# Optimization experiments

Hardware: AMD Instinct MI355X
Metric: run time of the kernel (lower is better)

## Reference

```python
import jax, jax.numpy as jnp
import numpy as np

B, L, H, E, FF, TOPK = 2, 2048, 1024, 8, 4096, 2

def setup_inputs() -> dict:
    key = jax.random.key(0)
    k1, k2, k3, k4 = jax.random.split(key, 4)
    scale = 1.0 / np.sqrt(H)
    x = jax.random.normal(k1, (B, L, H), dtype=jnp.float32)
    Wg = jax.random.normal(k2, (H, E), dtype=jnp.float32) * scale
    Wfc = jax.random.normal(k3, (E, H, FF), dtype=jnp.float32) * scale
    Wproj = jax.random.normal(k4, (E, FF, H), dtype=jnp.float32) * (1.0 / np.sqrt(FF))
    return {"x": x, "Wg": Wg, "Wfc": Wfc, "Wproj": Wproj, "topk": TOPK}

def reference(x, Wg, Wfc, Wproj, topk):
    b, l, h = x.shape
    e = Wg.shape[1]
    xf = x.reshape(-1, h)                      # [T, h]
    T = xf.shape[0]
    # --- router: softmax over experts, top-k select, renormalize ---
    probs = jax.nn.softmax(xf @ Wg, axis=-1)   # [T, E]
    sel_w, sel_e = jax.lax.top_k(probs, topk)  # [T, k]
    sel_w = sel_w / jnp.sum(sel_w, axis=-1, keepdims=True)
    # dense per-token expert weight matrix [T, E] (0 for unselected experts)
    dense_w = jnp.zeros((T, e), dtype=x.dtype).at[jnp.arange(T)[:, None], sel_e].add(sel_w)
    # --- experts: relu(x Wfc)^2 Wproj, combined with routing weights ---
    h1 = jnp.einsum('th,ehf->etf', xf, Wfc)    # [E, T, FF]
    h1 = jnp.square(jax.nn.relu(h1))
    y = jnp.einsum('etf,efh->eth', h1, Wproj)  # [E, T, h]
    out = jnp.einsum('eth,te->th', y, dense_w) # weighted combine
    return out.reshape(b, l, h)
```

## Files before the change

### kernel.cpp

```cpp
#include <hip/hip_runtime.h>

#define T_TOK 4096
#define HDIM  1024
#define NEXP  8
#define FFDIM 4096
#define NPAIR 8192
#define MAXMT 72

typedef __attribute__((ext_vector_type(8))) short short8;
typedef __attribute__((ext_vector_type(8))) unsigned short ushort8;
typedef __attribute__((ext_vector_type(4))) unsigned short ushort4_t;
typedef __attribute__((ext_vector_type(4))) float f32x4;

__device__ __forceinline__ unsigned short f2bf(float f) {
  unsigned int u = __float_as_uint(f);
  u += 0x7fffu + ((u >> 16) & 1u);
  return (unsigned short)(u >> 16);
}
__device__ __forceinline__ float bf2f(unsigned short u) {
  return __uint_as_float((unsigned int)u << 16);
}

__device__ __forceinline__ void gload16(const void* g, const void* l) {
  __builtin_amdgcn_global_load_lds(
      (const __attribute__((address_space(1))) unsigned int*)(unsigned long long)g,
      (__attribute__((address_space(3))) unsigned int*)(unsigned int)(unsigned long long)l,
      16, 0, 0);
}

__device__ __forceinline__ void transpose_tile_256(
    const float* __restrict__ in, unsigned short* __restrict__ out,
    int M, int N, int my, int nx, unsigned short* t , int tid) {
  int r0 = my * 256, c0 = nx * 64;
  int colb = (tid & 15) * 4;
  int rowi = tid >> 4;
  int sw = (tid & 7) << 3;
#pragma unroll
  for (int i = 0; i < 16; i++) {
    int row = i * 16 + rowi;
    float4 v = *(const float4*)(in + (size_t)(r0 + row) * N + c0 + colb);
    int rs = row ^ sw;
    t[(colb + 0) * 264 + rs] = f2bf(v.x);
    t[(colb + 1) * 264 + rs] = f2bf(v.y);
    t[(colb + 2) * 264 + rs] = f2bf(v.z);
    t[(colb + 3) * 264 + rs] = f2bf(v.w);
  }
  __syncthreads();
  int m0 = (tid & 31) * 8;
  int nsub = tid >> 5;
#pragma unroll
  for (int i = 0; i < 8; i++) {
    int n = i * 8 + nsub;
    int sn = ((n >> 2) & 7) << 3;
    ushort8 v = *(const ushort8*)&t[n * 264 + (m0 ^ sn)];
    *(ushort8*)(out + (size_t)(c0 + n) * M + r0 + m0) = v;
  }
}

__global__ __launch_bounds__(256) void routerA_kernel(
    const float* __restrict__ x, const float* __restrict__ wg,
    unsigned short* __restrict__ xb,
    int* __restrict__ sel_e, float* __restrict__ sel_w,
    const float* __restrict__ Wfc, unsigned short* __restrict__ WfcT) {
  __shared__ unsigned short tbuf[64 * 264];
  int id = blockIdx.x;
  if (id >= 1024) {
    int b = id - 1024;
    int e = b >> 8, r = b & 255;
    transpose_tile_256(Wfc + (size_t)e * HDIM * FFDIM, WfcT + (size_t)e * HDIM * FFDIM,
                       HDIM, FFDIM, r >> 6, r & 63, tbuf, threadIdx.x);
    return;
  }
  int lane = threadIdx.x & 63;
  int t = id * 4 + (threadIdx.x >> 6);
  const float* xr = x + (size_t)t * HDIM;
  unsigned short* xo = xb + (size_t)t * HDIM;
  float acc[8] = {0, 0, 0, 0, 0, 0, 0, 0};
#pragma unroll
  for (int i = 0; i < 4; i++) {
    int h0 = i * 256 + lane * 4;
    float4 xv = *(const float4*)(xr + h0);
    *(ushort4_t*)(xo + h0) = (ushort4_t){f2bf(xv.x), f2bf(xv.y), f2bf(xv.z), f2bf(xv.w)};
    float xs[4] = {xv.x, xv.y, xv.z, xv.w};
#pragma unroll
    for (int k = 0; k < 4; k++) {
      const float* wr_ = wg + (size_t)(h0 + k) * 8;
      float4 w0 = *(const float4*)(wr_);
      float4 w1 = *(const float4*)(wr_ + 4);
      acc[0] += xs[k] * w0.x; acc[1] += xs[k] * w0.y; acc[2] += xs[k] * w0.z; acc[3] += xs[k] * w0.w;
      acc[4] += xs[k] * w1.x; acc[5] += xs[k] * w1.y; acc[6] += xs[k] * w1.z; acc[7] += xs[k] * w1.w;
    }
  }
#pragma unroll
  for (int off = 32; off > 0; off >>= 1) {
#pragma unroll
    for (int e = 0; e < 8; e++) acc[e] += __shfl_xor(acc[e], off, 64);
  }
  if (lane == 0) {
    int e0 = 0; float b0 = acc[0];
#pragma unroll
    for (int e = 1; e < 8; e++) if (acc[e] > b0) { b0 = acc[e]; e0 = e; }
    int e1 = -1; float b1 = -3.4e38f;
#pragma unroll
    for (int e = 0; e < 8; e++) if (e != e0 && acc[e] > b1) { b1 = acc[e]; e1 = e; }
    float q = expf(b1 - b0);
    float w0 = 1.0f / (1.0f + q);
    float w1 = q / (1.0f + q);
    sel_e[t * 2] = e0; sel_e[t * 2 + 1] = e1;
    sel_w[t * 2] = w0; sel_w[t * 2 + 1] = w1;
  }
}

__global__ __launch_bounds__(1024) void count_scatter_kernel(
    const int* __restrict__ sel_e, int* __restrict__ counts,
    int* __restrict__ pair_token, int* __restrict__ pair_pos) {
  __shared__ int wtot[16][NEXP];
  __shared__ int wcur[16][NEXP];
  int tid = threadIdx.x;
  int wv = tid >> 6;
  int lane = tid & 63;
  int4 a = *(const int4*)(sel_e + tid * 8);
  int4 b = *(const int4*)(sel_e + tid * 8 + 4);
  int es[8] = {a.x, a.y, a.z, a.w, b.x, b.y, b.z, b.w};
  int c[NEXP] = {0, 0, 0, 0, 0, 0, 0, 0};
#pragma unroll
  for (int j = 0; j < 8; j++) c[es[j]]++;
#pragma unroll
  for (int off = 32; off > 0; off >>= 1)
#pragma unroll
    for (int e = 0; e < NEXP; e++) c[e] += __shfl_xor(c[e], off, 64);
  if (lane == 0)
#pragma unroll
    for (int e = 0; e < NEXP; e++) wtot[wv][e] = c[e];
  __syncthreads();
  if (tid == 0) {
    int tot[NEXP];
#pragma unroll
    for (int e = 0; e < NEXP; e++) {
      int s = 0;
      for (int w2 = 0; w2 < 16; w2++) s += wtot[w2][e];
      tot[e] = s;
    }
    int s = 0;
    for (int e = 0; e < NEXP; e++) {
      counts[e] = tot[e];
      int base = s;
      for (int w2 = 0; w2 < 16; w2++) { wcur[w2][e] = base; base += wtot[w2][e]; }
      s += tot[e];
    }
  }
  __syncthreads();
#pragma unroll
  for (int j = 0; j < 8; j++) {
    int e = es[j];
    int pos = atomicAdd(&wcur[wv][e], 1);
    int entry = tid * 8 + j;
    pair_token[pos] = entry >> 1;
    pair_pos[entry] = pos;
  }
}

__global__ __launch_bounds__(256) void combine_kernel(
    const unsigned short* __restrict__ y,
    const int* __restrict__ pair_pos, const float* __restrict__ sel_w,
    float* __restrict__ out) {
  int i = blockIdx.x * 256 + threadIdx.x;
  int t = i >> 7;
  int c = (i & 127) * 8;
  int p0 = pair_pos[t * 2], p1 = pair_pos[t * 2 + 1];
  float w0 = sel_w[t * 2], w1 = sel_w[t * 2 + 1];
  const unsigned short* y1p = y + (size_t)NPAIR * HDIM;
  ushort8 a0 = *(const ushort8*)(y + (size_t)p0 * HDIM + c);
  ushort8 b0 = *(const ushort8*)(y1p + (size_t)p0 * HDIM + c);
  ushort8 a1 = *(const ushort8*)(y + (size_t)p1 * HDIM + c);
  ushort8 b1 = *(const ushort8*)(y1p + (size_t)p1 * HDIM + c);
  float r[8];
#pragma unroll
  for (int j = 0; j < 8; j++)
    r[j] = w0 * (bf2f(a0[j]) + bf2f(b0[j])) + w1 * (bf2f(a1[j]) + bf2f(b1[j]));
  float4 v0 = {r[0], r[1], r[2], r[3]};
  float4 v1 = {r[4], r[5], r[6], r[7]};
  float* op = out + (size_t)t * HDIM + c;
  *(float4*)op = v0;
  *(float4*)(op + 4) = v1;
}

template <int KD, int KSPL, int NTP, bool GATHER, bool SQRELU, bool FUSET>
__global__ __launch_bounds__(512, 4) void moe_gemm_kernel(
    const unsigned short* __restrict__ A0, const unsigned short* __restrict__ B0,
    const int* __restrict__ counts, const int* __restrict__ pair_token,
    unsigned short* __restrict__ Cout,
    const float* __restrict__ tin, unsigned short* __restrict__ tout) {
  constexpr int ND = SQRELU ? FFDIM : HDIM;
  constexpr int KLEN = KD / KSPL;
  constexpr int NTILES = KLEN / 32;
  constexpr int NBG = NTP * KSPL * MAXMT;

  __shared__ char lds[73728];

  if (FUSET && blockIdx.x >= (unsigned)NBG) {
    int half = threadIdx.x >> 8;
    int tau = (blockIdx.x - NBG) * 2 + half;
    int e = tau >> 8, r = tau & 255;
    unsigned short* tb = (unsigned short*)lds + half * (64 * 264);
    transpose_tile_256(tin + (size_t)e * FFDIM * HDIM, tout + (size_t)e * FFDIM * HDIM,
                       FFDIM, HDIM, r >> 4, r & 15, tb, threadIdx.x & 255);
    return;
  }

  int d = blockIdx.x;
  int w = (d & 7) * (NBG >> 3) + (d >> 3);
  int nt = w % NTP;
  int rest = w / NTP;
  int ks = rest % KSPL;
  int mt = rest / KSPL;

  int eSel = -1, tloc = 0, segstart = 0, segcnt = 0;
  {
    int cumt = 0, acc = 0;
#pragma unroll
    for (int ee = 0; ee < NEXP; ee++) {
      int c = counts[ee];
      int ntl = (c + 127) >> 7;
      if (eSel < 0 && mt < cumt + ntl) { eSel = ee; tloc = mt - cumt; segstart = acc; segcnt = c; }
      cumt += ntl; acc += c;
    }
  }
  if (eSel < 0) return;

  if (!SQRELU) Cout += (size_t)ks * NPAIR * HDIM;

  const unsigned short* B = B0 + (size_t)eSel * ND * KD + (size_t)ks * KLEN;
  const unsigned short* Abase = A0 + (size_t)ks * KLEN;

  int tid = threadIdx.x;
  int lane = tid & 63;
  int wv = tid >> 6;
  int wr = wv >> 2;
  int wc = wv & 3;
  int g  = lane >> 4;
  int lr = lane & 15;

  int srow = tid >> 2;
  int schunk = (tid & 3) ^ ((tid >> 3) & 3);
  const unsigned short* aP;
  const unsigned short* bP[2];
  {
    int idx = tloc * 128 + srow;
    if (idx >= segcnt) idx = segcnt - 1;
    int p = segstart + idx;
    size_t rowoff;
    if (GATHER) rowoff = (size_t)pair_token[p] * KD;
    else        rowoff = (size_t)p * KD;
    aP = Abase + rowoff + schunk * 8;
#pragma unroll
    for (int r = 0; r < 2; r++)
      bP[r] = B + (size_t)(nt * 256 + r * 128 + srow) * KD + schunk * 8;
  }

  const char* ldsc = lds;
  int ldsW = wv * 1024;

  f32x4 acc[4][4];
#pragma unroll
  for (int i = 0; i < 4; i++)
#pragma unroll
    for (int j = 0; j < 4; j++) acc[i][j] = (f32x4){0.f, 0.f, 0.f, 0.f};

  int swz = (g ^ ((lr >> 1) & 3)) * 16;
  int abase0 = (wr * 64 + lr) * 64 + swz;
  int bbase0 = 8192 + (wc * 64 + lr) * 64 + swz;

#pragma unroll
  for (int t = 0; t < 2; t++) {
    int so = t * 24576;
    gload16(aP, ldsc + so + ldsW);
    gload16(bP[0], ldsc + so + 8192 + ldsW);
    gload16(bP[1], ldsc + so + 16384 + ldsW);
    aP += 32; bP[0] += 32; bP[1] += 32;
  }

  int rsOff = 0, rs2Off = 49152;
  for (int t = 0; t < NTILES; ++t) {
    if (t < NTILES - 1) {
      asm volatile("s_waitcnt vmcnt(3)" ::: "memory");
    } else {
      asm volatile("s_waitcnt vmcnt(0)" ::: "memory");
    }
    __builtin_amdgcn_s_barrier();
    __builtin_amdgcn_sched_barrier(0);

    short8 af[4], bf[4];
#pragma unroll
    for (int mi = 0; mi < 4; mi++)
      af[mi] = *(const short8*)(ldsc + rsOff + abase0 + mi * 1024);
#pragma unroll
    for (int nj = 0; nj < 4; nj++)
      bf[nj] = *(const short8*)(ldsc + rsOff + bbase0 + nj * 1024);

    if (t + 2 < NTILES) {
      gload16(aP, ldsc + rs2Off + ldsW);
      gload16(bP[0], ldsc + rs2Off + 8192 + ldsW);
      gload16(bP[1], ldsc + rs2Off + 16384 + ldsW);
      aP += 32; bP[0] += 32; bP[1] += 32;
    }

    __builtin_amdgcn_s_setprio(1);
#pragma unroll
    for (int mi = 0; mi < 4; mi++)
#pragma unroll
      for (int nj = 0; nj < 4; nj++)
        acc[mi][nj] = __builtin_amdgcn_mfma_f32_16x16x32_bf16(af[mi], bf[nj], acc[mi][nj], 0, 0, 0);
    __builtin_amdgcn_s_setprio(0);

    rsOff  = (rsOff  == 49152) ? 0 : rsOff  + 24576;
    rs2Off = (rs2Off == 49152) ? 0 : rs2Off + 24576;
  }

  __syncthreads();
  unsigned short* t2 = (unsigned short*)lds;
#pragma unroll
  for (int mi = 0; mi < 4; mi++) {
#pragma unroll
    for (int q = 0; q < 4; q++) {
      int row = wr * 64 + mi * 16 + g * 4 + q;
#pragma unroll
      for (int nj = 0; nj < 4; nj++) {
        int col = wc * 64 + nj * 16 + lr;
        float v = acc[mi][nj][q];
        if (SQRELU) v = v > 0.f ? v * v : 0.f;
        t2[row * 260 + col] = f2bf(v);
      }
    }
  }
  __syncthreads();
  {
    int row = tid >> 2;
    int idx = tloc * 128 + row;
    if (idx < segcnt) {
      size_t base = (size_t)(segstart + idx) * ND + nt * 256;
      const unsigned short* src = t2 + row * 260;
#pragma unroll
      for (int i = 0; i < 16; i++) {
        int c = ((tid & 3) + i * 4) * 4;
        *(ushort4_t*)(Cout + base + c) = *(const ushort4_t*)(src + c);
      }
    }
  }
}


extern "C" void kernel_launch(void* const* d_in, const int* in_sizes, int n_in,
                              void* d_out, int out_size, void* d_ws, size_t ws_size,
                              hipStream_t stream) {
  (void)in_sizes; (void)n_in; (void)out_size; (void)ws_size;
  const float* x     = (const float*)d_in[0];
  const float* Wg    = (const float*)d_in[1];
  const float* Wfc   = (const float*)d_in[2];
  const float* Wproj = (const float*)d_in[3];
  float* out = (float*)d_out;

  char* w = (char*)d_ws;
  size_t o = 0;
  auto take = [&](size_t n) { char* p = w + o; o += (n + 255) & ~(size_t)255; return p; };
  unsigned short* xb     = (unsigned short*)take((size_t)T_TOK * HDIM * 2);
  unsigned short* WfcT   = (unsigned short*)take((size_t)NEXP * FFDIM * HDIM * 2);
  unsigned short* WprojT = (unsigned short*)take((size_t)NEXP * HDIM * FFDIM * 2);
  unsigned short* h1     = (unsigned short*)take((size_t)NPAIR * FFDIM * 2);
  unsigned short* y      = (unsigned short*)take((size_t)2 * NPAIR * HDIM * 2);
  int*   sel_e      = (int*)take(T_TOK * 2 * 4);
  float* sel_w      = (float*)take(T_TOK * 2 * 4);
  int*   pair_token = (int*)take(NPAIR * 4);
  int*   pair_pos   = (int*)take(NPAIR * 4);
  int*   counts     = (int*)take(8 * 4);

  routerA_kernel<<<3072, 256, 0, stream>>>(x, Wg, xb, sel_e, sel_w, Wfc, WfcT);
  count_scatter_kernel<<<1, 1024, 0, stream>>>(sel_e, counts, pair_token, pair_pos);

  moe_gemm_kernel<HDIM, 1, FFDIM / 256, true, true, true>
      <<<(FFDIM / 256) * MAXMT + 1024, 512, 0, stream>>>(
          xb, WfcT, counts, pair_token, h1, Wproj, WprojT);
  moe_gemm_kernel<FFDIM, 2, HDIM / 256, false, false, false>
      <<<(HDIM / 256) * 2 * MAXMT, 512, 0, stream>>>(
          h1, WprojT, counts, pair_token, y, nullptr, nullptr);
  combine_kernel<<<T_TOK * (HDIM / 8) / 256, 256, 0, stream>>>(y, pair_pos, sel_w, out);
}
```

Baseline: 287.6 us.

## Load B operand fragments directly from global into registers, bypassing LDS

Weight (B) fragments are now read by each wave straight from global memory into registers, double-buffered across tiles. Only the A activations are still staged through an LDS triple buffer, so the LDS footprint and per-tile LDS traffic shrink. The cost is that B is fetched separately by both wave rows. Each lane's loads are narrow strided rows, so coalescing is poorer and the loop depends more on global-load latency being hidden by one tile of prefetch.

```diff
diff --git a/kernel.cpp b/kernel.cpp
--- a/kernel.cpp
+++ b/kernel.cpp
@@ -196,7 +196,7 @@
   constexpr int NTILES = KLEN / 32;
   constexpr int NBG = NTP * KSPL * MAXMT;
 
-  __shared__ char lds[73728];
+  __shared__ char lds[67584];
 
   if (FUSET && blockIdx.x >= (unsigned)NBG) {
     int half = threadIdx.x >> 8;
@@ -244,7 +244,6 @@
   int srow = tid >> 2;
   int schunk = (tid & 3) ^ ((tid >> 3) & 3);
   const unsigned short* aP;
-  const unsigned short* bP[2];
   {
     int idx = tloc * 128 + srow;
     if (idx >= segcnt) idx = segcnt - 1;
@@ -253,10 +252,8 @@
     if (GATHER) rowoff = (size_t)pair_token[p] * KD;
     else        rowoff = (size_t)p * KD;
     aP = Abase + rowoff + schunk * 8;
-#pragma unroll
-    for (int r = 0; r < 2; r++)
-      bP[r] = B + (size_t)(nt * 256 + r * 128 + srow) * KD + schunk * 8;
-  }
+  }
+  const unsigned short* bGlob = B + (size_t)(nt * 256 + wc * 64 + lr) * KD + g * 8;
 
   const char* ldsc = lds;
   int ldsW = wv * 1024;
@@ -269,40 +266,43 @@
 
   int swz = (g ^ ((lr >> 1) & 3)) * 16;
   int abase0 = (wr * 64 + lr) * 64 + swz;
-  int bbase0 = 8192 + (wc * 64 + lr) * 64 + swz;
-
-#pragma unroll
-  for (int t = 0; t < 2; t++) {
-    int so = t * 24576;
-    gload16(aP, ldsc + so + ldsW);
-    gload16(bP[0], ldsc + so + 8192 + ldsW);
-    gload16(bP[1], ldsc + so + 16384 + ldsW);
-    aP += 32; bP[0] += 32; bP[1] += 32;
-  }
-
-  int rsOff = 0, rs2Off = 49152;
-  for (int t = 0; t < NTILES; ++t) {
+
+  short8 bfA[4], bfB[4];
+
+  gload16(aP, ldsc + ldsW);
+  aP += 32;
+  asm volatile("" ::: "memory");
+#pragma unroll
+  for (int nj = 0; nj < 4; nj++)
+    bfA[nj] = *(const short8*)(bGlob + (size_t)nj * 16 * KD);
+  asm volatile("" ::: "memory");
+  gload16(aP, ldsc + 8192 + ldsW);
+  aP += 32;
+
+  int rsOff = 0, rs2Off = 16384;
+  auto step = [&](int t, short8 (&bcur)[4], short8 (&bnxt)[4]) {
     if (t < NTILES - 1) {
-      asm volatile("s_waitcnt vmcnt(3)" ::: "memory");
+      asm volatile("s_waitcnt vmcnt(1)" ::: "memory");
     } else {
       asm volatile("s_waitcnt vmcnt(0)" ::: "memory");
     }
     __builtin_amdgcn_s_barrier();
     __builtin_amdgcn_sched_barrier(0);
 
-    short8 af[4], bf[4];
+    short8 af[4];
 #pragma unroll
     for (int mi = 0; mi < 4; mi++)
       af[mi] = *(const short8*)(ldsc + rsOff + abase0 + mi * 1024);
-#pragma unroll
-    for (int nj = 0; nj < 4; nj++)
-      bf[nj] = *(const short8*)(ldsc + rsOff + bbase0 + nj * 1024);
-
+
+    if (t + 1 < NTILES) {
+#pragma unroll
+      for (int nj = 0; nj < 4; nj++)
+        bnxt[nj] = *(const short8*)(bGlob + (size_t)nj * 16 * KD + (t + 1) * 32);
+    }
+    asm volatile("" ::: "memory");
     if (t + 2 < NTILES) {
       gload16(aP, ldsc + rs2Off + ldsW);
-      gload16(bP[0], ldsc + rs2Off + 8192 + ldsW);
-      gload16(bP[1], ldsc + rs2Off + 16384 + ldsW);
-      aP += 32; bP[0] += 32; bP[1] += 32;
+      aP += 32;
     }
 
     __builtin_amdgcn_s_setprio(1);
@@ -310,11 +310,16 @@
     for (int mi = 0; mi < 4; mi++)
 #pragma unroll
       for (int nj = 0; nj < 4; nj++)
-        acc[mi][nj] = __builtin_amdgcn_mfma_f32_16x16x32_bf16(af[mi], bf[nj], acc[mi][nj], 0, 0, 0);
+        acc[mi][nj] = __builtin_amdgcn_mfma_f32_16x16x32_bf16(af[mi], bcur[nj], acc[mi][nj], 0, 0, 0);
     __builtin_amdgcn_s_setprio(0);
 
-    rsOff  = (rsOff  == 49152) ? 0 : rsOff  + 24576;
-    rs2Off = (rs2Off == 49152) ? 0 : rs2Off + 24576;
+    rsOff  = (rsOff  == 16384) ? 0 : rsOff  + 8192;
+    rs2Off = (rs2Off == 16384) ? 0 : rs2Off + 8192;
+  };
+
+  for (int tt = 0; tt < NTILES; tt += 2) {
+    step(tt, bfA, bfB);
+    step(tt + 1, bfB, bfA);
   }
 
   __syncthreads();
```

Result: slower. 488.3 us (+69.8%).
